# Kernel tuning notes

Hardware: AMD Instinct MI355X
Metric: run time of the kernel (lower is better)

Reference implementation:

```python
import jax, jax.numpy as jnp
import numpy as np

K_TEMP = 1.0  # swta softmax inverse temperature (init arg k)
KH = KW = 3
STRIDE = (1, 1)


def setup_inputs() -> dict:
    key = jax.random.key(0)
    k1, k2 = jax.random.split(key)
    B, C, H, W, O = 32, 64, 64, 64, 128
    x = jax.random.normal(k1, (B, C, H, W), dtype=jnp.float32)
    # xavier_normal_: std = sqrt(2 / (fan_in + fan_out)), fan = C*kh*kw / O*kh*kw
    fan_in = C * KH * KW
    fan_out = O * KH * KW
    std = float(np.sqrt(2.0 / (fan_in + fan_out)))
    weight = jax.random.normal(k2, (O, C, KH, KW), dtype=jnp.float32) * std
    bias = jnp.zeros((O,), dtype=jnp.float32)
    return {"x": x, "weight": weight, "bias": bias}


def _normalize_w(weight):
    nrm = jnp.sqrt(jnp.sum(weight * weight, axis=(1, 2, 3), keepdims=True))
    nrm = jnp.where(nrm == 0, jnp.ones_like(nrm), nrm)
    return weight / nrm


def reference(x, weight, bias):
    O = weight.shape[0]
    # forward: conv2d with L2-normalized filters + bias (act = Identity)
    w = _normalize_w(weight)
    y = jax.lax.conv_general_dilated(
        x, w, window_strides=STRIDE, padding='VALID',
        dimension_numbers=('NCHW', 'OIHW', 'NCHW'))
    y = y + bias[None, :, None, None]  # (B, O, Hp, Wp)

    # swta patchwise Hebbian update -> delta_w (torch: no_grad buffer)
    # im2col, channel-major patch ordering (c, kh, kw) matches F.unfold
    patches = jax.lax.conv_general_dilated_patches(
        x, filter_shape=(KH, KW), window_strides=STRIDE, padding='VALID')  # (B, C*KH*KW, Hp, Wp)
    Bn, CK, Hp, Wp = patches.shape
    x_unf = patches.transpose(0, 2, 3, 1).reshape(Bn * Hp * Wp, CK)  # (B*L, C*KH*KW)

    r = jax.nn.softmax(y * K_TEMP, axis=1).transpose(1, 0, 2, 3)  # (O, B, Hp, Wp)
    r_abs = jnp.abs(r)
    r_sum = jnp.sum(r_abs, axis=(1, 2, 3), keepdims=True)
    r_sum = jnp.where(r_sum == 0, jnp.ones_like(r_sum), r_sum)
    cr = (r_abs / r_sum) * r  # (O, B, Hp, Wp)
    cr_mat = cr.reshape(O, -1)  # (O, B*L)

    dec = jnp.sum(cr_mat, axis=1, keepdims=True) * weight.reshape(O, -1)
    delta_w = (cr_mat @ x_unf - dec).reshape(weight.shape)
    return y, delta_w
```

## Files before the change

kernel.cpp:

```cpp
#include <hip/hip_runtime.h>

#define Bn 32
#define Cn 64
#define Hn 64
#define Wn 64
#define On 128
#define HP 62
#define WP 62
#define CKn 576
#define Ln (HP*WP)
#define Y_ELEMS (Bn*On*Ln)

typedef unsigned int uint32;
typedef unsigned short ushort16;
typedef __bf16 bf16x8 __attribute__((ext_vector_type(8)));
typedef float floatx4 __attribute__((ext_vector_type(4)));

static __device__ __forceinline__ uint32 bf16r(float f){
  uint32 u = __float_as_uint(f);
  return (u + 0x7FFFu + ((u >> 16) & 1u)) >> 16;
}

#define KSB   4
#define GSZ   (On*CKn)
#define NS1   0
#define NS2   128
#define NG    256
#define NWNB  (NG + KSB*GSZ)
#define NXB   (NWNB + 36864)
#define NPB   (NXB + 4194304)
#define WS_NEED ((size_t)49800000)

__global__ __launch_bounds__(256) void k_norm(const float* __restrict__ w, ushort16* __restrict__ wnb,
                                              float* __restrict__ S1, float* __restrict__ S2,
                                              float* __restrict__ G, int ngbuf){
  int o = blockIdx.x; int t = threadIdx.x;
  for (int kq = 0; kq < ngbuf; kq++)
    for (int k = t; k < CKn; k += 256) G[(size_t)kq*GSZ + o*CKn + k] = 0.f;
  if (t == 0){ S1[o] = 0.f; S2[o] = 0.f; }
  float s = 0.f;
  for (int k = t; k < CKn; k += 256){ float v = w[o*CKn + k]; s += v*v; }
  #pragma unroll
  for (int off = 32; off; off >>= 1) s += __shfl_down(s, off);
  __shared__ float red[4]; __shared__ float sh_inv;
  if ((t & 63) == 0) red[t >> 6] = s;
  __syncthreads();
  if (t == 0){
    float tot = red[0] + red[1] + red[2] + red[3];
    float nrm = sqrtf(tot);
    sh_inv = (nrm == 0.f) ? 1.f : 1.f/nrm;
  }
  __syncthreads();
  float inv = sh_inv;
  for (int k = t; k < CKn; k += 256){
    float v = w[o*CKn + k] * inv;
    int c = k / 9;
    int q = k - c*9;
    wnb[o*CKn + q*64 + c] = (ushort16)bf16r(v);
  }
}

__global__ __launch_bounds__(256) void k_xb(const float* __restrict__ x, ushort16* __restrict__ xb){
  size_t idx = ((size_t)blockIdx.x*256 + threadIdx.x)*4;
  float4 v = *(const float4*)(x + idx);
  uint2 o;
  o.x = bf16r(v.x) | (bf16r(v.y) << 16);
  o.y = bf16r(v.z) | (bf16r(v.w) << 16);
  *(uint2*)(xb + idx) = o;
}

__global__ __launch_bounds__(256, 3) void k_convm(const float* __restrict__ x,
                                                  const ushort16* __restrict__ wnb,
                                                  const float* __restrict__ bias,
                                                  float* __restrict__ y){
  __shared__ ushort16 slab[4*64*68];
  __shared__ ushort16 Bl[2][128*36];
  int t = threadIdx.x;
  int lane = t & 63;
  int wv = t >> 6;
  int mtile = blockIdx.x;
  int b = blockIdx.y;
  int i0 = mtile*2;
  {
    int c0 = (t & 31)*2;
    int grp = t >> 5;
    int r = grp >> 1;
    int w0 = (grp & 1)*32;
    const float* p0 = x + (((size_t)b*Cn + c0)*Hn + (i0 + r))*Wn + w0;
    const float* p1 = p0 + (size_t)Hn*Wn;
    #pragma unroll
    for (int ch = 0; ch < 4; ch++){
      float4 A0 = *(const float4*)(p0 + ch*8);
      float4 A1 = *(const float4*)(p0 + ch*8 + 4);
      float4 B0 = *(const float4*)(p1 + ch*8);
      float4 B1 = *(const float4*)(p1 + ch*8 + 4);
      float v0[8] = {A0.x,A0.y,A0.z,A0.w,A1.x,A1.y,A1.z,A1.w};
      float v1[8] = {B0.x,B0.y,B0.z,B0.w,B1.x,B1.y,B1.z,B1.w};
      #pragma unroll
      for (int qq = 0; qq < 8; qq++){
        int wloc = w0 + ch*8 + qq;
        *(uint32*)&slab[(r*64 + wloc)*68 + c0] = (bf16r(v1[qq]) << 16) | bf16r(v0[qq]);
      }
    }
  }
  int ob = t >> 1;
  int kh16 = (t & 1)*16;
  const ushort16* wrow = wnb + (size_t)ob*CKn + kh16;
  {
    uint4 bA = *(const uint4*)(wrow);
    uint4 bB = *(const uint4*)(wrow + 8);
    ushort16* dst = &Bl[0][ob*36 + kh16];
    ((uint2*)dst)[0] = make_uint2(bA.x, bA.y);
    ((uint2*)dst)[1] = make_uint2(bA.z, bA.w);
    ((uint2*)dst)[2] = make_uint2(bB.x, bB.y);
    ((uint2*)dst)[3] = make_uint2(bB.z, bB.w);
  }
  int quad8 = (lane >> 4) << 3;
  int iT[2], jT[2];
  #pragma unroll
  for (int mt = 0; mt < 2; mt++){
    int m = wv*32 + mt*16 + (lane & 15);
    int pos = m < 124 ? m : 123;
    int hi = pos >= 62;
    iT[mt] = hi;
    jT[mt] = pos - (hi ? 62 : 0);
  }
  floatx4 acc[2][8];
  #pragma unroll
  for (int mt = 0; mt < 2; mt++)
    #pragma unroll
    for (int nt = 0; nt < 8; nt++)
      acc[mt][nt] = (floatx4){0.f, 0.f, 0.f, 0.f};
  union U8 { uint2 u[2]; bf16x8 v; };
  for (int s = 0; s < 18; s++){
    uint4 nA, nB;
    if (s < 17){
      nA = *(const uint4*)(wrow + (s+1)*32);
      nB = *(const uint4*)(wrow + (s+1)*32 + 8);
    }
    __syncthreads();
    int k0 = s*32 + quad8;
    int q = k0 >> 6;
    int c0 = k0 & 63;
    int kh = (q*86) >> 8;
    int kw = q - kh*3;
    bf16x8 af[2];
    #pragma unroll
    for (int mt = 0; mt < 2; mt++){
      const ushort16* ap = &slab[((iT[mt] + kh)*64 + jT[mt] + kw)*68 + c0];
      U8 ua;
      ua.u[0] = *(const uint2*)(ap);
      ua.u[1] = *(const uint2*)(ap + 4);
      af[mt] = ua.v;
    }
    const ushort16* bbase = &Bl[s & 1][(lane & 15)*36 + quad8];
    bf16x8 bf[8];
    #pragma unroll
    for (int nt = 0; nt < 8; nt++){
      const ushort16* bp = bbase + nt*576;
      U8 ub;
      ub.u[0] = *(const uint2*)(bp);
      ub.u[1] = *(const uint2*)(bp + 4);
      bf[nt] = ub.v;
    }
    #pragma unroll
    for (int mt = 0; mt < 2; mt++)
      #pragma unroll
      for (int nt = 0; nt < 8; nt++)
        acc[mt][nt] = __builtin_amdgcn_mfma_f32_16x16x32_bf16(af[mt], bf[nt], acc[mt][nt], 0, 0, 0);
    if (s < 17){
      ushort16* dst = &Bl[(s+1) & 1][ob*36 + kh16];
      ((uint2*)dst)[0] = make_uint2(nA.x, nA.y);
      ((uint2*)dst)[1] = make_uint2(nA.z, nA.w);
      ((uint2*)dst)[2] = make_uint2(nB.x, nB.y);
      ((uint2*)dst)[3] = make_uint2(nB.z, nB.w);
    }
  }
  float bv[8];
  #pragma unroll
  for (int nt = 0; nt < 8; nt++) bv[nt] = bias[nt*16 + (lane & 15)];
  float* ytile = (float*)slab;
  int cl = lane & 15;
  int quad = lane >> 4;
  #pragma unroll
  for (int chunk = 0; chunk < 2; chunk++){
    __syncthreads();
    #pragma unroll
    for (int nt4 = 0; nt4 < 4; nt4++){
      int nt = chunk*4 + nt4;
      int ol = nt4*16 + cl;
      #pragma unroll
      for (int mt = 0; mt < 2; mt++){
        #pragma unroll
        for (int reg = 0; reg < 4; reg++){
          int m = wv*32 + mt*16 + quad*4 + reg;
          if (m < 124) ytile[ol*130 + m] = acc[mt][nt][reg] + bv[nt];
        }
      }
    }
    __syncthreads();
    #pragma unroll
    for (int r = 0; r < 16; r++){
      int ol = wv*16 + r;
      int o = chunk*64 + ol;
      if (lane < 62){
        float2 v = *(float2*)&ytile[ol*130 + lane*2];
        *(float2*)&y[((size_t)b*On + o)*Ln + (size_t)i0*WP + lane*2] = v;
      }
    }
  }
}

__global__ __launch_bounds__(256, 4) void k_softp(const float* __restrict__ y, ushort16* __restrict__ pb,
                                                  float* __restrict__ S1, float* __restrict__ S2){
  __shared__ float mpart[2][256], dpart[2][256];
  __shared__ float s1loc[128], s2loc[128];
  int b = blockIdx.x;
  int s = blockIdx.y;
  int i0 = s*2;
  int t = threadIdx.x;
  int j = t & 63;
  int og = t >> 6;
  if (t < 128){ s1loc[t] = 0.f; s2loc[t] = 0.f; }
  int je = j < WP ? j : (WP-1);
  const float* yb = y + ((size_t)b*On + og*32)*Ln + (size_t)i0*WP + je;
  float v0[32], v1[32];
  #pragma unroll
  for (int oi = 0; oi < 32; oi++){
    const float* yp = yb + (size_t)oi*Ln;
    v0[oi] = yp[0];
    v1[oi] = yp[WP];
  }
  float m0 = v0[0], m1 = v1[0];
  #pragma unroll
  for (int oi = 1; oi < 32; oi++){
    m0 = fmaxf(m0, v0[oi]);
    m1 = fmaxf(m1, v1[oi]);
  }
  float d0 = 0.f, d1 = 0.f;
  #pragma unroll
  for (int oi = 0; oi < 32; oi++){
    v0[oi] = __expf(v0[oi] - m0); d0 += v0[oi];
    v1[oi] = __expf(v1[oi] - m1); d1 += v1[oi];
  }
  mpart[0][t] = m0; dpart[0][t] = d0;
  mpart[1][t] = m1; dpart[1][t] = d1;
  __syncthreads();
  float scl[2];
  {
    float ml[2] = {m0, m1};
    #pragma unroll
    for (int r = 0; r < 2; r++){
      float ma = mpart[r][j],      mb = mpart[r][64+j];
      float mcc = mpart[r][128+j], md = mpart[r][192+j];
      float mm = fmaxf(fmaxf(ma, mb), fmaxf(mcc, md));
      float dd = dpart[r][j]*__expf(ma-mm) + dpart[r][64+j]*__expf(mb-mm)
               + dpart[r][128+j]*__expf(mcc-mm) + dpart[r][192+j]*__expf(md-mm);
      scl[r] = __expf(ml[r]-mm) / dd;
    }
  }
  bool act = j < WP;
  float sc0 = act ? scl[0] : 0.f;
  float sc1 = act ? scl[1] : 0.f;
  ushort16* ppb = pb + (((size_t)b*On + og*32)*HP + i0)*64 + j;
  #pragma unroll
  for (int oi = 0; oi < 32; oi++){
    float r0 = v0[oi]*sc0;
    float r1 = v1[oi]*sc1;
    float p0 = r0*r0, p1 = r1*r1;
    ushort16* pp = ppb + (size_t)oi*(HP*64);
    pp[0]  = (ushort16)bf16r(p0);
    pp[64] = (ushort16)bf16r(p1);
    float s1v = r0 + r1, s2v = p0 + p1;
    #pragma unroll
    for (int off = 32; off; off >>= 1){ s1v += __shfl_down(s1v, off); s2v += __shfl_down(s2v, off); }
    if (j == 0){ s1loc[og*32 + oi] += s1v; s2loc[og*32 + oi] += s2v; }
  }
  __syncthreads();
  if (t < 128){ atomicAdd(&S1[t], s1loc[t]); atomicAdd(&S2[t], s2loc[t]); }
}

#define DOKH2(av, dc, ec, off) { \
  U16 f0, f1, f2; \
  f0.q = dc; \
  f1.q = make_uint4((dc.x>>16)|(dc.y<<16), (dc.y>>16)|(dc.z<<16), \
                    (dc.z>>16)|(dc.w<<16), (dc.w>>16)|(ec<<16)); \
  f2.q = make_uint4(dc.y, dc.z, dc.w, ec); \
  acc[(off)+0] = __builtin_amdgcn_mfma_f32_16x16x32_bf16(av, f0.v, acc[(off)+0], 0, 0, 0); \
  acc[(off)+1] = __builtin_amdgcn_mfma_f32_16x16x32_bf16(av, f1.v, acc[(off)+1], 0, 0, 0); \
  acc[(off)+2] = __builtin_amdgcn_mfma_f32_16x16x32_bf16(av, f2.v, acc[(off)+2], 0, 0, 0); \
}

__global__ __launch_bounds__(512, 2) void k_deltam(const ushort16* __restrict__ xb,
                                                   const ushort16* __restrict__ pb,
                                                   float* __restrict__ G){
  __shared__ uint4 lds4[36864/16];
  char* ldsb = (char*)lds4;
  int t = threadIdx.x;
  int lane = t & 63;
  int wv = t >> 6;
  int mgl = wv & 3;
  int ih  = wv >> 2;
  int bx  = blockIdx.x;
  int ntk = bx & 3;
  int khalf = bx >> 2;
  int b   = blockIdx.y;
  int oh  = blockIdx.z;
  int it0 = khalf*16;
  int nit = khalf ? 15 : 16;
  int cl = lane & 15;
  int quad = lane >> 4;
  int quad8 = quad << 3;

  int o128 = t >> 2;
  int sP = o128 >> 6;
  int oP = o128 & 63;
  int segP = t & 3;
  const ushort16* pbase = pb + ((size_t)b*On + oh*64 + oP)*(HP*64) + segP*16;
  int pIrow = sP*31 + it0;
  char* pwr = ldsb + (sP*64 + oP)*128;
  int psw0 = ((2*segP)     ^ (oP & 7)) << 4;
  int psw1 = ((2*segP + 1) ^ (oP & 7)) << 4;
  int pX = t & 7;
  int r1 = t >> 3;
  int s1_ = (r1 >= 48) ? 1 : 0;
  int rr1 = r1 - s1_*48;
  int c1 = rr1/3, kh1 = rr1 - c1*3;
  int rr2 = (64 + (t >> 3)) - 48;
  int c2 = rr2/3, kh2 = rr2 - c2*3;
  const ushort16* xbb = xb + ((size_t)b*Cn + ntk*16)*(Hn*Wn) + pX*8;
  const ushort16* x1base = xbb + (size_t)c1*(Hn*Wn);
  const ushort16* x2base = xbb + (size_t)c2*(Hn*Wn);
  int x1Irow = s1_*31 + kh1 + it0;
  int x2Irow = 31 + kh2 + it0;
  char* x1wr = ldsb + 16384 + (s1_*48 + c1*3 + kh1)*144 + pX*16;
  char* x2wr = ldsb + 16384 + (48    + c2*3 + kh2)*144 + pX*16;

  if (t < 96) *(uint4*)(ldsb + 16384 + t*144 + 128) = make_uint4(0,0,0,0);

  const char* ptb = ldsb + ih*8192;
  const char* xtb = ldsb + 16384 + ih*6912;
  int orow = mgl*16 + cl;
  int o7 = cl & 7;

  floatx4 acc[9];
  #pragma unroll
  for (int nt = 0; nt < 9; nt++) acc[nt] = (floatx4){0.f, 0.f, 0.f, 0.f};
  union U16 { uint4 q; bf16x8 v; };

  uint4 pr0, pr1, xr0, xr1;
  {
    const ushort16* prow = pbase + (size_t)(pIrow + 0)*64;
    pr0 = *(const uint4*)(prow);
    pr1 = *(const uint4*)(prow + 8);
    xr0 = *(const uint4*)(x1base + (size_t)(x1Irow + 0)*Wn);
    if (t < 256) xr1 = *(const uint4*)(x2base + (size_t)(x2Irow + 0)*Wn);
  }

  for (int it = 0; it < nit; ++it){
    __syncthreads();
    *(uint4*)(pwr + psw0) = pr0;
    *(uint4*)(pwr + psw1) = pr1;
    *(uint4*)(x1wr) = xr0;
    if (t < 256) *(uint4*)(x2wr) = xr1;
    if (it < nit-1){
      const ushort16* prow = pbase + (size_t)(pIrow + it + 1)*64;
      pr0 = *(const uint4*)(prow);
      pr1 = *(const uint4*)(prow + 8);
      xr0 = *(const uint4*)(x1base + (size_t)(x1Irow + it + 1)*Wn);
      if (t < 256) xr1 = *(const uint4*)(x2base + (size_t)(x2Irow + it + 1)*Wn);
    }
    __syncthreads();
    #pragma unroll
    for (int sl = 0; sl < 2; sl++){
      U16 a;
      a.q = *(const uint4*)(ptb + orow*128 + (((sl*4 + quad) ^ o7) << 4));
      #pragma unroll
      for (int kh = 0; kh < 3; kh++){
        const char* rb = xtb + (cl*3 + kh)*144;
        uint4 d = *(const uint4*)(rb + ((sl*32 + quad8) << 1));
        uint32 e = *(const uint32*)(rb + ((sl*32 + quad8 + 8) << 1));
        DOKH2(a.v, d, e, kh*3)
      }
    }
  }

  __syncthreads();
  float* sc = (float*)ldsb;
  if (ih == 1){
    #pragma unroll
    for (int nt = 0; nt < 9; nt++)
      #pragma unroll
      for (int reg = 0; reg < 4; reg++)
        sc[(mgl*16 + quad*4 + reg)*144 + nt*16 + cl] = acc[nt][reg];
  }
  __syncthreads();
  if (ih == 0){
    float* Gq = G + (size_t)(b & 3)*GSZ;
    #pragma unroll
    for (int nt = 0; nt < 9; nt++)
      #pragma unroll
      for (int reg = 0; reg < 4; reg++){
        int ol = mgl*16 + quad*4 + reg;
        int og = oh*64 + ol;
        float v = acc[nt][reg] + sc[ol*144 + nt*16 + cl];
        atomicAdd(&Gq[(size_t)og*CKn + nt*64 + ntk*16 + cl], v);
      }
  }
}

__global__ __launch_bounds__(576) void k_finalm(const float* __restrict__ w, const float* __restrict__ G,
                                                const float* __restrict__ S1, const float* __restrict__ S2,
                                                float* __restrict__ dw){
  int o = blockIdx.x; int k = threadIdx.x;
  int c = k / 9;
  int q = k - c*9;
  float s1 = S1[o]; if (s1 == 0.f) s1 = 1.f;
  float g = 0.f;
  #pragma unroll
  for (int kq = 0; kq < KSB; kq++) g += G[(size_t)kq*GSZ + o*CKn + q*64 + c];
  dw[o*CKn + k] = (g - S2[o]*w[o*CKn + k]) / s1;
}

__global__ __launch_bounds__(256) void k_soft_old(const float* __restrict__ y, float* __restrict__ mbuf,
                                                  float* __restrict__ invdbuf, float* __restrict__ S1,
                                                  float* __restrict__ S2){
  __shared__ float s1loc[128], s2loc[128];
  int t = threadIdx.x;
  if (t < 128){ s1loc[t] = 0.f; s2loc[t] = 0.f; }
  __syncthreads();
  int b = blockIdx.x;
  int i = blockIdx.y*4 + (t >> 6);
  int j = t & 63;
  bool act = (i < 62) && (j < 62);
  const float* yp = y + (((size_t)b*On)*HP + (i < 62 ? i : 0))*WP + j;
  float mx = -3.0e38f;
  if (act){ for (int o = 0; o < On; o++) mx = fmaxf(mx, yp[(size_t)o*Ln]); }
  float den = 0.f;
  if (act){ for (int o = 0; o < On; o++) den += __expf(yp[(size_t)o*Ln] - mx); }
  float inv = act ? 1.f/den : 0.f;
  if (act){
    int pos = (b*HP + i)*WP + j;
    mbuf[pos] = mx; invdbuf[pos] = inv;
  }
  for (int o = 0; o < On; o++){
    float r = act ? __expf(yp[(size_t)o*Ln] - mx)*inv : 0.f;
    float s1v = r, s2v = r*r;
    #pragma unroll
    for (int off = 32; off; off >>= 1){ s1v += __shfl_down(s1v, off); s2v += __shfl_down(s2v, off); }
    if ((t & 63) == 0){ atomicAdd(&s1loc[o], s1v); atomicAdd(&s2loc[o], s2v); }
  }
  __syncthreads();
  if (t < 128){ atomicAdd(&S1[t], s1loc[t]); atomicAdd(&S2[t], s2loc[t]); }
}

__global__ __launch_bounds__(256) void k_delta_old(const float* __restrict__ x, const float* __restrict__ y,
                                                   const float* __restrict__ mbuf, const float* __restrict__ invdbuf,
                                                   float* __restrict__ G){
  __shared__ float planes[3][64][64];
  __shared__ float plds[16][64];
  int o0 = blockIdx.x * 16;
  int bs = blockIdx.y;
  int b = bs >> 2;
  int s = bs & 3;
  int i0 = s * 16;
  int nrows = (s == 3) ? 14 : 16;
  int t = threadIdx.x;
  int lane = t & 63;
  int w = t >> 6;
  int lc = t >> 2;
  int lw0 = (t & 3) << 4;
  const float* xb = x + (size_t)b*(Cn*Hn*Wn) + (size_t)lc*(Hn*Wn) + lw0;
  float acc[4][9];
  #pragma unroll
  for (int oi = 0; oi < 4; oi++)
    #pragma unroll
    for (int q = 0; q < 9; q++) acc[oi][q] = 0.f;
  #pragma unroll
  for (int pp = 0; pp < 2; pp++){
    int ih = i0 + pp;
    const float* src = xb + (size_t)ih*Wn;
    #pragma unroll
    for (int q = 0; q < 16; q++) planes[ih % 3][lw0 + q][lc] = src[q];
  }
  for (int ii = 0; ii < nrows; ii++){
    int i = i0 + ii;
    {
      int ih = i + 2;
      const float* src = xb + (size_t)ih*Wn;
      #pragma unroll
      for (int q = 0; q < 16; q++) planes[ih % 3][lw0 + q][lc] = src[q];
    }
    int R = b*HP + i;
    #pragma unroll
    for (int oi = 0; oi < 4; oi++){
      int o = o0 + w*4 + oi;
      float p = 0.f;
      if (lane < WP){
        int pos = R*WP + lane;
        float yv = y[(((size_t)b*On + o)*HP + i)*WP + lane];
        float r = __expf(yv - mbuf[pos]) * invdbuf[pos];
        p = r*r;
      }
      plds[w*4 + oi][lane] = p;
    }
    __syncthreads();
    int c = lane;
    int s0 = i % 3, s1 = (i+1) % 3, s2g = (i+2) % 3;
    #pragma unroll 1
    for (int jj0 = 0; jj0 < 56; jj0 += 8){
      float xv[3][12];
      #pragma unroll
      for (int q = 0; q < 12; q++){
        xv[0][q] = planes[s0][jj0+q][c];
        xv[1][q] = planes[s1][jj0+q][c];
        xv[2][q] = planes[s2g][jj0+q][c];
      }
      #pragma unroll
      for (int oi = 0; oi < 4; oi++){
        float4 pa = *(const float4*)&plds[w*4+oi][jj0];
        float4 pbq = *(const float4*)&plds[w*4+oi][jj0+4];
        float pv[8] = {pa.x,pa.y,pa.z,pa.w,pbq.x,pbq.y,pbq.z,pbq.w};
        #pragma unroll
        for (int kh = 0; kh < 3; kh++)
          #pragma unroll
          for (int kw = 0; kw < 3; kw++)
            #pragma unroll
            for (int dj = 0; dj < 8; dj++)
              acc[oi][kh*3+kw] += pv[dj]*xv[kh][dj+kw];
      }
    }
    {
      float xv[3][12];
      #pragma unroll
      for (int q = 0; q < 12; q++){
        bool ok = (56 + q) < 64;
        xv[0][q] = ok ? planes[s0][56+q][c] : 0.f;
        xv[1][q] = ok ? planes[s1][56+q][c] : 0.f;
        xv[2][q] = ok ? planes[s2g][56+q][c] : 0.f;
      }
      #pragma unroll
      for (int oi = 0; oi < 4; oi++){
        float4 pa = *(const float4*)&plds[w*4+oi][56];
        float4 pbq = *(const float4*)&plds[w*4+oi][60];
        float pv[8] = {pa.x,pa.y,pa.z,pa.w,pbq.x,pbq.y,pbq.z,pbq.w};
        #pragma unroll
        for (int kh = 0; kh < 3; kh++)
          #pragma unroll
          for (int kw = 0; kw < 3; kw++)
            #pragma unroll
            for (int dj = 0; dj < 8; dj++)
              acc[oi][kh*3+kw] += pv[dj]*xv[kh][dj+kw];
      }
    }
    __syncthreads();
  }
  #pragma unroll
  for (int oi = 0; oi < 4; oi++){
    float* Gr = G + (size_t)(o0 + w*4 + oi)*CKn + lane*9;
    #pragma unroll
    for (int q = 0; q < 9; q++) atomicAdd(&Gr[q], acc[oi][q]);
  }
}

__global__ __launch_bounds__(576) void k_final_old(const float* __restrict__ w, const float* __restrict__ G,
                                                   const float* __restrict__ S1, const float* __restrict__ S2,
                                                   float* __restrict__ dw){
  int o = blockIdx.x; int k = threadIdx.x;
  float s1 = S1[o]; if (s1 == 0.f) s1 = 1.f;
  dw[o*CKn + k] = (G[o*CKn + k] - S2[o]*w[o*CKn + k]) / s1;
}

extern "C" void kernel_launch(void* const* d_in, const int* in_sizes, int n_in,
                              void* d_out, int out_size, void* d_ws, size_t ws_size,
                              hipStream_t stream){
  const float* x    = (const float*)d_in[0];
  const float* w    = (const float*)d_in[1];
  const float* bias = (const float*)d_in[2];
  float* y  = (float*)d_out;
  float* dw = (float*)d_out + Y_ELEMS;
  float* ws = (float*)d_ws;

  if (ws_size >= WS_NEED){
    float* S1 = ws + NS1;
    float* S2 = ws + NS2;
    float* G  = ws + NG;
    ushort16* wnb = (ushort16*)(ws + NWNB);
    ushort16* xb  = (ushort16*)(ws + NXB);
    ushort16* pb  = (ushort16*)(ws + NPB);
    k_norm  <<<dim3(On),      dim3(256), 0, stream>>>(w, wnb, S1, S2, G, KSB);
    k_xb    <<<dim3(8192),    dim3(256), 0, stream>>>(x, xb);
    k_convm <<<dim3(31, Bn),  dim3(256), 0, stream>>>(x, wnb, bias, y);
    k_softp <<<dim3(Bn, 31),  dim3(256), 0, stream>>>(y, pb, S1, S2);
    k_deltam<<<dim3(8, Bn, 2), dim3(512), 0, stream>>>(xb, pb, G);
    k_finalm<<<dim3(On),      dim3(CKn), 0, stream>>>(w, G, S1, S2, dw);
  } else {
    float* S1   = ws + 73728;
    float* S2   = ws + 73856;
    float* G    = ws + 73984;
    float* mbuf = ws + 147712;
    float* invd = ws + 270720;
    ushort16* wnb = (ushort16*)(ws + 393728);
    k_norm     <<<dim3(On),      dim3(256), 0, stream>>>(w, wnb, S1, S2, G, 1);
    k_convm    <<<dim3(31, Bn),  dim3(256), 0, stream>>>(x, wnb, bias, y);
    k_soft_old <<<dim3(Bn, 16),  dim3(256), 0, stream>>>(y, mbuf, invd, S1, S2);
    k_delta_old<<<dim3(8, Bn*4), dim3(256), 0, stream>>>(x, y, mbuf, invd, G);
    k_final_old<<<dim3(On),      dim3(CKn), 0, stream>>>(w, G, S1, S2, dw);
  }
}
```

Baseline: 224.9 us.

## Cover all 128 outputs per delta block to reuse im2col x tiles

The delta-weight GEMM kernel now has each block compute all 128 output channels instead of splitting them across two blocks in the grid's z dimension. Each loaded x tile feeds two MFMA A operands, so x global loads and LDS staging are halved per output. The cost is double the accumulator registers, more LDS (46.5KB), launch bounds lowered to one block per CU, and half as many blocks. Occupancy and latency hiding drop in exchange.

```diff
diff --git a/kernel.cpp b/kernel.cpp
--- a/kernel.cpp
+++ b/kernel.cpp
@@ -280,21 +280,24 @@
   if (t < 128){ atomicAdd(&S1[t], s1loc[t]); atomicAdd(&S2[t], s2loc[t]); }
 }
 
-#define DOKH2(av, dc, ec, off) { \
+#define DOKH3(a0, a1, dc, ec, off) { \
   U16 f0, f1, f2; \
   f0.q = dc; \
   f1.q = make_uint4((dc.x>>16)|(dc.y<<16), (dc.y>>16)|(dc.z<<16), \
                     (dc.z>>16)|(dc.w<<16), (dc.w>>16)|(ec<<16)); \
   f2.q = make_uint4(dc.y, dc.z, dc.w, ec); \
-  acc[(off)+0] = __builtin_amdgcn_mfma_f32_16x16x32_bf16(av, f0.v, acc[(off)+0], 0, 0, 0); \
-  acc[(off)+1] = __builtin_amdgcn_mfma_f32_16x16x32_bf16(av, f1.v, acc[(off)+1], 0, 0, 0); \
-  acc[(off)+2] = __builtin_amdgcn_mfma_f32_16x16x32_bf16(av, f2.v, acc[(off)+2], 0, 0, 0); \
-}
-
-__global__ __launch_bounds__(512, 2) void k_deltam(const ushort16* __restrict__ xb,
+  acc[0][(off)+0] = __builtin_amdgcn_mfma_f32_16x16x32_bf16(a0, f0.v, acc[0][(off)+0], 0, 0, 0); \
+  acc[1][(off)+0] = __builtin_amdgcn_mfma_f32_16x16x32_bf16(a1, f0.v, acc[1][(off)+0], 0, 0, 0); \
+  acc[0][(off)+1] = __builtin_amdgcn_mfma_f32_16x16x32_bf16(a0, f1.v, acc[0][(off)+1], 0, 0, 0); \
+  acc[1][(off)+1] = __builtin_amdgcn_mfma_f32_16x16x32_bf16(a1, f1.v, acc[1][(off)+1], 0, 0, 0); \
+  acc[0][(off)+2] = __builtin_amdgcn_mfma_f32_16x16x32_bf16(a0, f2.v, acc[0][(off)+2], 0, 0, 0); \
+  acc[1][(off)+2] = __builtin_amdgcn_mfma_f32_16x16x32_bf16(a1, f2.v, acc[1][(off)+2], 0, 0, 0); \
+}
+
+__global__ __launch_bounds__(512, 1) void k_deltam(const ushort16* __restrict__ xb,
                                                    const ushort16* __restrict__ pb,
                                                    float* __restrict__ G){
-  __shared__ uint4 lds4[36864/16];
+  __shared__ uint4 lds4[46592/16];
   char* ldsb = (char*)lds4;
   int t = threadIdx.x;
   int lane = t & 63;
@@ -305,22 +308,22 @@
   int ntk = bx & 3;
   int khalf = bx >> 2;
   int b   = blockIdx.y;
-  int oh  = blockIdx.z;
   int it0 = khalf*16;
   int nit = khalf ? 15 : 16;
   int cl = lane & 15;
   int quad = lane >> 4;
   int quad8 = quad << 3;
 
-  int o128 = t >> 2;
-  int sP = o128 >> 6;
-  int oP = o128 & 63;
-  int segP = t & 3;
-  const ushort16* pbase = pb + ((size_t)b*On + oh*64 + oP)*(HP*64) + segP*16;
+  int o256 = t >> 1;
+  int sP = o256 >> 7;
+  int oP = o256 & 127;
+  int segP = t & 1;
+  const ushort16* pbase = pb + ((size_t)b*On + oP)*(HP*64) + segP*32;
   int pIrow = sP*31 + it0;
-  char* pwr = ldsb + (sP*64 + oP)*128;
-  int psw0 = ((2*segP)     ^ (oP & 7)) << 4;
-  int psw1 = ((2*segP + 1) ^ (oP & 7)) << 4;
+  char* pwr = ldsb + (sP*128 + oP)*128;
+  int psw[4];
+  #pragma unroll
+  for (int jj = 0; jj < 4; jj++) psw[jj] = ((4*segP + jj) ^ (oP & 7)) << 4;
   int pX = t & 7;
   int r1 = t >> 3;
   int s1_ = (r1 >= 48) ? 1 : 0;
@@ -333,79 +336,85 @@
   const ushort16* x2base = xbb + (size_t)c2*(Hn*Wn);
   int x1Irow = s1_*31 + kh1 + it0;
   int x2Irow = 31 + kh2 + it0;
-  char* x1wr = ldsb + 16384 + (s1_*48 + c1*3 + kh1)*144 + pX*16;
-  char* x2wr = ldsb + 16384 + (48    + c2*3 + kh2)*144 + pX*16;
-
-  if (t < 96) *(uint4*)(ldsb + 16384 + t*144 + 128) = make_uint4(0,0,0,0);
-
-  const char* ptb = ldsb + ih*8192;
-  const char* xtb = ldsb + 16384 + ih*6912;
+  char* x1wr = ldsb + 32768 + (s1_*48 + c1*3 + kh1)*144 + pX*16;
+  char* x2wr = ldsb + 32768 + (48    + c2*3 + kh2)*144 + pX*16;
+
+  if (t < 96) *(uint4*)(ldsb + 32768 + t*144 + 128) = make_uint4(0,0,0,0);
+
+  const char* ptb = ldsb + ih*16384;
+  const char* xtb = ldsb + 32768 + ih*6912;
   int orow = mgl*16 + cl;
   int o7 = cl & 7;
 
-  floatx4 acc[9];
-  #pragma unroll
-  for (int nt = 0; nt < 9; nt++) acc[nt] = (floatx4){0.f, 0.f, 0.f, 0.f};
+  floatx4 acc[2][9];
+  #pragma unroll
+  for (int h = 0; h < 2; h++)
+    #pragma unroll
+    for (int nt = 0; nt < 9; nt++) acc[h][nt] = (floatx4){0.f, 0.f, 0.f, 0.f};
   union U16 { uint4 q; bf16x8 v; };
 
-  uint4 pr0, pr1, xr0, xr1;
+  uint4 pr[4], xr0, xr1;
   {
     const ushort16* prow = pbase + (size_t)(pIrow + 0)*64;
-    pr0 = *(const uint4*)(prow);
-    pr1 = *(const uint4*)(prow + 8);
+    #pragma unroll
+    for (int jj = 0; jj < 4; jj++) pr[jj] = *(const uint4*)(prow + jj*8);
     xr0 = *(const uint4*)(x1base + (size_t)(x1Irow + 0)*Wn);
     if (t < 256) xr1 = *(const uint4*)(x2base + (size_t)(x2Irow + 0)*Wn);
   }
 
   for (int it = 0; it < nit; ++it){
     __syncthreads();
-    *(uint4*)(pwr + psw0) = pr0;
-    *(uint4*)(pwr + psw1) = pr1;
+    #pragma unroll
+    for (int jj = 0; jj < 4; jj++) *(uint4*)(pwr + psw[jj]) = pr[jj];
     *(uint4*)(x1wr) = xr0;
     if (t < 256) *(uint4*)(x2wr) = xr1;
     if (it < nit-1){
       const ushort16* prow = pbase + (size_t)(pIrow + it + 1)*64;
-      pr0 = *(const uint4*)(prow);
-      pr1 = *(const uint4*)(prow + 8);
+      #pragma unroll
+      for (int jj = 0; jj < 4; jj++) pr[jj] = *(const uint4*)(prow + jj*8);
       xr0 = *(const uint4*)(x1base + (size_t)(x1Irow + it + 1)*Wn);
       if (t < 256) xr1 = *(const uint4*)(x2base + (size_t)(x2Irow + it + 1)*Wn);
     }
     __syncthreads();
     #pragma unroll
     for (int sl = 0; sl < 2; sl++){
-      U16 a;
-      a.q = *(const uint4*)(ptb + orow*128 + (((sl*4 + quad) ^ o7) << 4));
+      int g16 = ((sl*4 + quad) ^ o7) << 4;
+      U16 a0, a1;
+      a0.q = *(const uint4*)(ptb + orow*128 + g16);
+      a1.q = *(const uint4*)(ptb + (64 + orow)*128 + g16);
       #pragma unroll
       for (int kh = 0; kh < 3; kh++){
         const char* rb = xtb + (cl*3 + kh)*144;
         uint4 d = *(const uint4*)(rb + ((sl*32 + quad8) << 1));
         uint32 e = *(const uint32*)(rb + ((sl*32 + quad8 + 8) << 1));
-        DOKH2(a.v, d, e, kh*3)
-      }
-    }
-  }
-
-  __syncthreads();
+        DOKH3(a0.v, a1.v, d, e, kh*3)
+      }
+    }
+  }
+
   float* sc = (float*)ldsb;
-  if (ih == 1){
-    #pragma unroll
-    for (int nt = 0; nt < 9; nt++)
-      #pragma unroll
-      for (int reg = 0; reg < 4; reg++)
-        sc[(mgl*16 + quad*4 + reg)*144 + nt*16 + cl] = acc[nt][reg];
-  }
-  __syncthreads();
-  if (ih == 0){
-    float* Gq = G + (size_t)(b & 3)*GSZ;
-    #pragma unroll
-    for (int nt = 0; nt < 9; nt++)
-      #pragma unroll
-      for (int reg = 0; reg < 4; reg++){
-        int ol = mgl*16 + quad*4 + reg;
-        int og = oh*64 + ol;
-        float v = acc[nt][reg] + sc[ol*144 + nt*16 + cl];
-        atomicAdd(&Gq[(size_t)og*CKn + nt*64 + ntk*16 + cl], v);
-      }
+  float* Gq = G + (size_t)(b & 3)*GSZ;
+  #pragma unroll
+  for (int half = 0; half < 2; half++){
+    __syncthreads();
+    if (ih == 1){
+      #pragma unroll
+      for (int nt = 0; nt < 9; nt++)
+        #pragma unroll
+        for (int reg = 0; reg < 4; reg++)
+          sc[(mgl*16 + quad*4 + reg)*144 + nt*16 + cl] = acc[half][nt][reg];
+    }
+    __syncthreads();
+    if (ih == 0){
+      #pragma unroll
+      for (int nt = 0; nt < 9; nt++)
+        #pragma unroll
+        for (int reg = 0; reg < 4; reg++){
+          int ol = mgl*16 + quad*4 + reg;
+          float v = acc[half][nt][reg] + sc[ol*144 + nt*16 + cl];
+          atomicAdd(&Gq[(size_t)(half*64 + ol)*CKn + nt*64 + ntk*16 + cl], v);
+        }
+    }
   }
 }
 
@@ -592,7 +601,7 @@
     k_xb    <<<dim3(8192),    dim3(256), 0, stream>>>(x, xb);
     k_convm <<<dim3(31, Bn),  dim3(256), 0, stream>>>(x, wnb, bias, y);
     k_softp <<<dim3(Bn, 31),  dim3(256), 0, stream>>>(y, pb, S1, S2);
-    k_deltam<<<dim3(8, Bn, 2), dim3(512), 0, stream>>>(xb, pb, G);
+    k_deltam<<<dim3(8, Bn),   dim3(512), 0, stream>>>(xb, pb, G);
     k_finalm<<<dim3(On),      dim3(CKn), 0, stream>>>(w, G, S1, S2, dw);
   } else {
     float* S1   = ws + 73728;
```

After: 251.7 us. +11.9%, slower.

## Merge weight-norm and x-to-bf16 kernels; XOR-swizzle x tile in delta kernel LDS

Applied to the files above, without the earlier changes.

Combines the weight normalization kernel and the x bf16 conversion kernel into one launch, with a block-index split deciding which job each block does. This removes one kernel launch and its gap. In the delta kernel, the x slab in LDS changes from padded 144-byte rows to 128-byte rows with an XOR swizzle on the 16-byte chunk index, which is meant to avoid bank conflicts and shrink LDS use. The padding zero-fill is dropped, and the boundary chunk read is replaced by a conditional zero, which adds a branch to the inner loop.

```diff
diff --git a/kernel.cpp b/kernel.cpp
--- a/kernel.cpp
+++ b/kernel.cpp
@@ -31,6 +31,47 @@
 #define NPB   (NXB + 4194304)
 #define WS_NEED ((size_t)49800000)
 
+__global__ __launch_bounds__(256) void k_normxb(const float* __restrict__ w, ushort16* __restrict__ wnb,
+                                                float* __restrict__ S1, float* __restrict__ S2,
+                                                float* __restrict__ G,
+                                                const float* __restrict__ x, ushort16* __restrict__ xbo){
+  __shared__ float red[4]; __shared__ float sh_inv;
+  int bid = blockIdx.x;
+  int t = threadIdx.x;
+  if (bid < 8192){
+    size_t idx = ((size_t)bid*256 + t)*4;
+    float4 v = *(const float4*)(x + idx);
+    uint2 o;
+    o.x = bf16r(v.x) | (bf16r(v.y) << 16);
+    o.y = bf16r(v.z) | (bf16r(v.w) << 16);
+    *(uint2*)(xbo + idx) = o;
+    return;
+  }
+  int o = bid - 8192;
+  for (int kq = 0; kq < KSB; kq++)
+    for (int k = t; k < CKn; k += 256) G[(size_t)kq*GSZ + o*CKn + k] = 0.f;
+  if (t == 0){ S1[o] = 0.f; S2[o] = 0.f; }
+  float s = 0.f;
+  for (int k = t; k < CKn; k += 256){ float v = w[o*CKn + k]; s += v*v; }
+  #pragma unroll
+  for (int off = 32; off; off >>= 1) s += __shfl_down(s, off);
+  if ((t & 63) == 0) red[t >> 6] = s;
+  __syncthreads();
+  if (t == 0){
+    float tot = red[0] + red[1] + red[2] + red[3];
+    float nrm = sqrtf(tot);
+    sh_inv = (nrm == 0.f) ? 1.f : 1.f/nrm;
+  }
+  __syncthreads();
+  float inv = sh_inv;
+  for (int k = t; k < CKn; k += 256){
+    float v = w[o*CKn + k] * inv;
+    int c = k / 9;
+    int q = k - c*9;
+    wnb[o*CKn + q*64 + c] = (ushort16)bf16r(v);
+  }
+}
+
 __global__ __launch_bounds__(256) void k_norm(const float* __restrict__ w, ushort16* __restrict__ wnb,
                                               float* __restrict__ S1, float* __restrict__ S2,
                                               float* __restrict__ G, int ngbuf){
@@ -58,15 +99,6 @@
     int q = k - c*9;
     wnb[o*CKn + q*64 + c] = (ushort16)bf16r(v);
   }
-}
-
-__global__ __launch_bounds__(256) void k_xb(const float* __restrict__ x, ushort16* __restrict__ xb){
-  size_t idx = ((size_t)blockIdx.x*256 + threadIdx.x)*4;
-  float4 v = *(const float4*)(x + idx);
-  uint2 o;
-  o.x = bf16r(v.x) | (bf16r(v.y) << 16);
-  o.y = bf16r(v.z) | (bf16r(v.w) << 16);
-  *(uint2*)(xb + idx) = o;
 }
 
 __global__ __launch_bounds__(256, 3) void k_convm(const float* __restrict__ x,
@@ -310,7 +342,6 @@
   int nit = khalf ? 15 : 16;
   int cl = lane & 15;
   int quad = lane >> 4;
-  int quad8 = quad << 3;
 
   int o128 = t >> 2;
   int sP = o128 >> 6;
@@ -333,13 +364,11 @@
   const ushort16* x2base = xbb + (size_t)c2*(Hn*Wn);
   int x1Irow = s1_*31 + kh1 + it0;
   int x2Irow = 31 + kh2 + it0;
-  char* x1wr = ldsb + 16384 + (s1_*48 + c1*3 + kh1)*144 + pX*16;
-  char* x2wr = ldsb + 16384 + (48    + c2*3 + kh2)*144 + pX*16;
-
-  if (t < 96) *(uint4*)(ldsb + 16384 + t*144 + 128) = make_uint4(0,0,0,0);
+  char* x1wr = ldsb + 16384 + (s1_*48 + c1*3 + kh1)*128 + ((pX ^ ((c1*3+kh1)&7))<<4);
+  char* x2wr = ldsb + 16384 + (48    + c2*3 + kh2)*128 + ((pX ^ ((c2*3+kh2)&7))<<4);
 
   const char* ptb = ldsb + ih*8192;
-  const char* xtb = ldsb + 16384 + ih*6912;
+  const char* xtb = ldsb + 16384 + ih*6144;
   int orow = mgl*16 + cl;
   int o7 = cl & 7;
 
@@ -377,9 +406,12 @@
       a.q = *(const uint4*)(ptb + orow*128 + (((sl*4 + quad) ^ o7) << 4));
       #pragma unroll
       for (int kh = 0; kh < 3; kh++){
-        const char* rb = xtb + (cl*3 + kh)*144;
-        uint4 d = *(const uint4*)(rb + ((sl*32 + quad8) << 1));
-        uint32 e = *(const uint32*)(rb + ((sl*32 + quad8 + 8) << 1));
+        int row = cl*3 + kh;
+        const char* rb = xtb + row*128;
+        int r7x = row & 7;
+        int g = sl*4 + quad;
+        uint4 d = *(const uint4*)(rb + ((g ^ r7x) << 4));
+        uint32 e = (g < 7) ? *(const uint32*)(rb + (((g+1) ^ r7x) << 4)) : 0u;
         DOKH2(a.v, d, e, kh*3)
       }
     }
@@ -588,8 +620,7 @@
     ushort16* wnb = (ushort16*)(ws + NWNB);
     ushort16* xb  = (ushort16*)(ws + NXB);
     ushort16* pb  = (ushort16*)(ws + NPB);
-    k_norm  <<<dim3(On),      dim3(256), 0, stream>>>(w, wnb, S1, S2, G, KSB);
-    k_xb    <<<dim3(8192),    dim3(256), 0, stream>>>(x, xb);
+    k_normxb<<<dim3(8320),    dim3(256), 0, stream>>>(w, wnb, S1, S2, G, x, xb);
     k_convm <<<dim3(31, Bn),  dim3(256), 0, stream>>>(x, wnb, bias, y);
     k_softp <<<dim3(Bn, 31),  dim3(256), 0, stream>>>(y, pb, S1, S2);
     k_deltam<<<dim3(8, Bn, 2), dim3(512), 0, stream>>>(xb, pb, G);
```

After: 209.6 us. 1.07x faster.
